# Optimization experiments

Measured on AMD Instinct MI355X. Metric: run time of the kernel, lower is better.

Reference implementation:

```python
import jax, jax.numpy as jnp
import numpy as np

C = 1024
H = 16
K = 2  # num_states
B, N = 4, 4096


def setup_inputs() -> dict:
    key = jax.random.key(0)
    ks_ = jax.random.split(key, 12)
    s = 1.0 / np.sqrt(C)
    inp = {
        "x": jax.random.normal(ks_[0], (B, N, C), dtype=jnp.float32),
        "Wq": jax.random.normal(ks_[1], (C, C), dtype=jnp.float32) * s,
        "bq": jnp.zeros((C,), dtype=jnp.float32),
        "Wk": jax.random.normal(ks_[2], (K, C, C), dtype=jnp.float32) * s,
        "bk": jnp.zeros((K, C), dtype=jnp.float32),
        "Wv": jax.random.normal(ks_[3], (K, C, C), dtype=jnp.float32) * s,
        "bv": jnp.zeros((K, C), dtype=jnp.float32),
        "Wo": jax.random.normal(ks_[4], (C, C), dtype=jnp.float32) * s,
        "bo": jnp.zeros((C,), dtype=jnp.float32),
        "ln_g": jnp.ones((C,), dtype=jnp.float32),
        "ln_b": jnp.zeros((C,), dtype=jnp.float32),
    }
    return inp


def _heads(t):
    # [..., n, (h d)] -> [..., h, n, d]
    shp = t.shape
    d = shp[-1] // H
    t = t.reshape(shp[:-1] + (H, d))
    return jnp.swapaxes(t, -2, -3)


def reference(x, Wq, bq, Wk, bk, Wv, bv, Wo, bo, ln_g, ln_b):
    dtype = x.dtype
    # residual single-layer projections (ResidualMLP with num_layers=-1)
    q = x + jnp.einsum('bnc,cd->bnd', x, Wq) + bq
    ks = x[None] + jnp.einsum('bnc,kcd->kbnd', x, Wk) + bk[:, None, None, :]
    vs = x[None] + jnp.einsum('bnc,kcd->kbnd', x, Wv) + bv[:, None, None, :]
    q = _heads(q)        # [b,h,n,d]
    ks = _heads(ks)      # [k,b,h,n,d]
    vs = _heads(vs)      # [k,b,h,n,d]
    scale = 1.0 / jnp.sqrt(jnp.asarray(N, dtype=jnp.float32))
    ks = ks.astype(jnp.float32) * scale
    vs = vs.astype(jnp.float32) * scale
    # per-state KV outer-products: [k,b,h,d,e]
    states = jnp.einsum('kbhnd,kbhne->kbhde', ks, vs)
    state = jnp.prod(states, axis=0)  # [b,h,d,e]
    out = jnp.einsum('bhnd,bhde->bhne', q.astype(jnp.float32), state)
    out = out.astype(dtype)
    # [b,h,n,d] -> [b,n,(h d)]
    out = jnp.swapaxes(out, 1, 2).reshape(x.shape[0], x.shape[1], C)
    # LayerNorm
    mu = jnp.mean(out, axis=-1, keepdims=True)
    var = jnp.var(out, axis=-1, keepdims=True)
    out = (out - mu) / jnp.sqrt(var + 1e-5) * ln_g + ln_b
    out = jnp.einsum('bnc,cd->bnd', out, Wo) + bo
    return out
```

## Files before the change

kernel.cpp:

```cpp
#include <hip/hip_runtime.h>
#include <hip/hip_bf16.h>

typedef __attribute__((ext_vector_type(8))) short bf16x8;
typedef __attribute__((ext_vector_type(4))) float f32x4;
typedef __attribute__((ext_vector_type(4))) short s16x4;

__device__ __forceinline__ short f2bf(float f) {
  union { float f; unsigned u; } v; v.f = f;
  unsigned r = v.u + 0x7fffu + ((v.u >> 16) & 1u);
  return (short)(r >> 16);
}

__device__ __forceinline__ float bf2f(short s) {
  union { float f; unsigned u; } v; v.u = ((unsigned)(unsigned short)s) << 16;
  return v.f;
}

#define GLD_LDS(g, l) __builtin_amdgcn_global_load_lds( \
    (const __attribute__((address_space(1))) void*)(g), \
    (__attribute__((address_space(3))) void*)(l), 16, 0, 0)

__global__ __launch_bounds__(256)
void convt_k(const float* __restrict__ x, short* __restrict__ xb,
             short* __restrict__ xbT, float* __restrict__ s) {
  __shared__ short tile[64][72];
  __shared__ float red[4][64];
  const int b = blockIdx.z;
  const int n0 = blockIdx.y * 64;
  const int c0 = blockIdx.x * 64;
  const int t = threadIdx.x;
  const int nl = t >> 4;
  const int c4 = (t & 15) << 2;
  const float* xp = x + ((size_t)b * 4096 + n0) * 1024 + c0;
#pragma unroll
  for (int i = 0; i < 4; ++i) {
    const int n = nl + 16 * i;
    const float4 v = *(const float4*)(xp + (size_t)n * 1024 + c4);
    s16x4 o;
    o[0] = f2bf(v.x); o[1] = f2bf(v.y); o[2] = f2bf(v.z); o[3] = f2bf(v.w);
    *(s16x4*)(&xb[((size_t)b * 4096 + n0 + n) * 1024 + c0 + c4]) = o;
    *(s16x4*)(&tile[n][c4]) = o;
  }
  __syncthreads();
  const int cll = t >> 4;
  const int n4 = (t & 15) << 2;
#pragma unroll
  for (int i = 0; i < 4; ++i) {
    const int c = cll + 16 * i;
    s16x4 o;
    o[0] = tile[n4 + 0][c]; o[1] = tile[n4 + 1][c];
    o[2] = tile[n4 + 2][c]; o[3] = tile[n4 + 3][c];
    *(s16x4*)(&xbT[((size_t)b * 1024 + c0 + c) * 4096 + n0 + n4]) = o;
  }
  const int part = t >> 6, col = t & 63;
  float cs = 0.f;
#pragma unroll
  for (int i = 0; i < 16; ++i) cs += bf2f(tile[part * 16 + i][col]);
  red[part][col] = cs;
  __syncthreads();
  if (part == 0)
    atomicAdd(&s[b * 1024 + c0 + col],
              red[0][col] + red[1][col] + red[2][col] + red[3][col]);
}

__global__ void twc_k(const float* __restrict__ Wq, const float* __restrict__ Wk,
                      const float* __restrict__ Wv, const float* __restrict__ Wo,
                      const float* __restrict__ lng, short* __restrict__ dst,
                      short* __restrict__ wqn) {
  __shared__ float tile[32][33];
  const int z = blockIdx.z;
  const float* src = (z == 0) ? Wq
                   : (z == 1) ? Wk
                   : (z == 2) ? (Wk + 1048576)
                   : (z == 3) ? Wv
                   : (z == 4) ? (Wv + 1048576)
                   : Wo;
  short* d = dst + (size_t)z * 1048576;
  const int tx = threadIdx.x, ty = threadIdx.y;
  const int c0 = blockIdx.y * 32, d0 = blockIdx.x * 32;
#pragma unroll
  for (int i = 0; i < 4; ++i) {
    const int cc = c0 + ty + i * 8;
    const float v = src[(size_t)cc * 1024 + d0 + tx];
    tile[ty + i * 8][tx] = v;
    if (z == 0)
      wqn[(size_t)cc * 1024 + d0 + tx] = f2bf(v + (cc == d0 + tx ? 1.0f : 0.0f));
  }
  __syncthreads();
#pragma unroll
  for (int i = 0; i < 4; ++i) {
    const int cc = c0 + tx;
    const int dd = d0 + ty + i * 8;
    float v = tile[tx][ty + i * 8];
    if (z < 5) {
      if (cc == dd) v += 1.0f;
    } else {
      v *= lng[cc];
    }
    d[(size_t)dd * 1024 + cc] = f2bf(v);
  }
}

__global__ __launch_bounds__(256)
void gemv_k(const short* __restrict__ wt, const float* __restrict__ s,
            float* __restrict__ u, float* __restrict__ w) {
  const int z = blockIdx.z, b = blockIdx.y;
  const int lane = threadIdx.x & 63, wid = threadIdx.x >> 6;
  const short* W = wt + ((size_t)(z + 1) << 20);
  const float* sb = s + b * 1024;
  float* outp = (z < 2) ? (u + (z * 4 + b) * 1024) : (w + ((z - 2) * 4 + b) * 1024);
#pragma unroll 1
  for (int it = 0; it < 16; ++it) {
    const int d = blockIdx.x * 64 + wid * 16 + it;
    const short* row = W + (size_t)d * 1024 + lane * 16;
    float acc = 0.f;
#pragma unroll
    for (int j = 0; j < 16; ++j) acc += bf2f(row[j]) * sb[lane * 16 + j];
#pragma unroll
    for (int o = 32; o > 0; o >>= 1) acc += __shfl_down(acc, o);
    if (lane == 0) outp[d] = acc;
  }
}

__global__ __launch_bounds__(256)
void ut_k(const float* __restrict__ Wo, const float* __restrict__ lng,
          const float* __restrict__ lnb, const float* __restrict__ bo,
          float* __restrict__ u, float* __restrict__ t) {
  const int dl = threadIdx.x & 63;
  const int dd = blockIdx.x * 64 + dl;
  const int part = threadIdx.x >> 6;
  float su = 0.f, st = 0.f;
  for (int c = part * 256; c < part * 256 + 256; ++c) {
    const float w = Wo[(size_t)c * 1024 + dd];
    su += lng[c] * w;
    st += lnb[c] * w;
  }
  __shared__ float rs[4][64], rt[4][64];
  rs[part][dl] = su; rt[part][dl] = st;
  __syncthreads();
  if (part == 0) {
    su = rs[0][dl] + rs[1][dl] + rs[2][dl] + rs[3][dl];
    st = rt[0][dl] + rt[1][dl] + rt[2][dl] + rt[3][dl];
    u[dd] = su;
    t[dd] = st + bo[dd];
  }
}

__global__ __launch_bounds__(512, 2)
void gram_k(const short* __restrict__ xbT, float* __restrict__ Pg) {
  extern __shared__ short lds[];
  const int tid = threadIdx.x;
  const int lane = tid & 63;
  const int wv = tid >> 6;
  const int wm = wv >> 2;
  const int wn = wv & 3;
  const int swz = ((blockIdx.x & 7) << 5) + (blockIdx.x >> 3);
  const int b = swz >> 6;
  const int kz = (swz >> 4) & 3;
  const int tl = swz & 15;
  const int bm0 = (tl >> 2) << 8, bn0 = (tl & 3) << 8;
  const int koff = kz << 10;
  const short* Ap = xbT + ((size_t)b << 22);
  float* po = Pg + ((size_t)((kz << 2) + b) << 20);

  const int lrow = ((lane >> 3) << 1) | ((lane >> 2) & 1);
  const int kc = ((lane & 3) ^ ((lane >> 3) & 3)) << 3;
  const int cl = lane & 15;
  const int khi = lane >> 4;

  f32x4 acc[8][4];
#pragma unroll
  for (int i = 0; i < 8; ++i)
#pragma unroll
    for (int j = 0; j < 4; ++j) acc[i][j] = f32x4{0.f, 0.f, 0.f, 0.f};

  auto stage = [&](int buf, int t) {
    const int k0 = koff + (t << 5) + kc;
    short* ab = lds + (buf << 14);
    short* bb = ab + 8192;
#pragma unroll
    for (int c = 0; c < 2; ++c) {
      const int un = wv * 2 + c;
      GLD_LDS(Ap + (size_t)(bm0 + (un << 4) + lrow) * 4096 + k0, ab + (un << 9));
      GLD_LDS(Ap + (size_t)(bn0 + (un << 4) + lrow) * 4096 + k0, bb + (un << 9));
    }
  };

  auto compute = [&](int buf) {
    const short* ab = lds + (buf << 14);
    const short* bb = ab + 8192;
    bf16x8 af[8], bfr[4];
#pragma unroll
    for (int i = 0; i < 8; ++i) {
      const int R = (wm << 7) + (i << 4) + cl;
      af[i] = *(const bf16x8*)(ab + (R << 5) + ((khi ^ ((R >> 1) & 3)) << 3));
    }
#pragma unroll
    for (int j = 0; j < 4; ++j) {
      const int C = (wn << 6) + (j << 4) + cl;
      bfr[j] = *(const bf16x8*)(bb + (C << 5) + ((khi ^ ((C >> 1) & 3)) << 3));
    }
#pragma unroll
    for (int i = 0; i < 8; ++i)
#pragma unroll
      for (int j = 0; j < 4; ++j)
        acc[i][j] = __builtin_amdgcn_mfma_f32_16x16x32_bf16(af[i], bfr[j], acc[i][j], 0, 0, 0);
  };

  stage(0, 0);
  stage(1, 1);
  asm volatile("s_waitcnt vmcnt(4)" ::: "memory");
  __builtin_amdgcn_s_barrier();
#pragma unroll 1
  for (int t = 0; t < 30; ++t) {
    stage((t + 2) & 3, t + 2);
    compute(t & 3);
    asm volatile("s_waitcnt vmcnt(4)" ::: "memory");
    __builtin_amdgcn_s_barrier();
  }
  compute(2);
  asm volatile("s_waitcnt vmcnt(0)" ::: "memory");
  __builtin_amdgcn_s_barrier();
  compute(3);

#pragma unroll
  for (int i = 0; i < 8; ++i)
#pragma unroll
    for (int j = 0; j < 4; ++j) {
      const int col = bn0 + (wn << 6) + (j << 4) + cl;
      const int rowb = bm0 + (wm << 7) + (i << 4) + (khi << 2);
#pragma unroll
      for (int r = 0; r < 4; ++r)
        po[(size_t)(rowb + r) * 1024 + col] = acc[i][j][r];
    }
}

__global__ __launch_bounds__(512, 2)
void oat_k(const short* __restrict__ xb, const short* __restrict__ Beff,
           const float* __restrict__ rq, short* __restrict__ oat,
           float* __restrict__ musum, float* __restrict__ sqsum) {
  extern __shared__ short lds[];
  const int tid = threadIdx.x;
  const int lane = tid & 63;
  const int wv = tid >> 6;
  const int wm = wv >> 2;
  const int wn = wv & 3;
  const int swz = ((blockIdx.x & 7) << 5) + (blockIdx.x >> 3);
  const int b = swz >> 6;
  const int tl = swz & 63;
  const int bm0 = (tl >> 2) << 8;
  const int bn0 = (tl & 3) << 8;
  const short* Ap = xb + ((size_t)b << 22);
  const short* Bp = Beff + ((size_t)b << 20);

  const int lrow = ((lane >> 3) << 1) | ((lane >> 2) & 1);
  const int kc = ((lane & 3) ^ ((lane >> 3) & 3)) << 3;
  const int cl = lane & 15;
  const int khi = lane >> 4;

  f32x4 acc[8][4];
#pragma unroll
  for (int i = 0; i < 8; ++i)
#pragma unroll
    for (int j = 0; j < 4; ++j) acc[i][j] = f32x4{0.f, 0.f, 0.f, 0.f};

  auto stage = [&](int buf, int t) {
    const int k0 = (t << 5) + kc;
    short* ab = lds + (buf << 14);
    short* bb = ab + 8192;
#pragma unroll
    for (int c = 0; c < 2; ++c) {
      const int un = wv * 2 + c;
      GLD_LDS(Ap + (size_t)(bm0 + (un << 4) + lrow) * 1024 + k0, ab + (un << 9));
      GLD_LDS(Bp + (size_t)(bn0 + (un << 4) + lrow) * 1024 + k0, bb + (un << 9));
    }
  };

  auto compute = [&](int buf) {
    const short* ab = lds + (buf << 14);
    const short* bb = ab + 8192;
    bf16x8 af[8], bfr[4];
#pragma unroll
    for (int i = 0; i < 8; ++i) {
      const int R = (wm << 7) + (i << 4) + cl;
      af[i] = *(const bf16x8*)(ab + (R << 5) + ((khi ^ ((R >> 1) & 3)) << 3));
    }
#pragma unroll
    for (int j = 0; j < 4; ++j) {
      const int C = (wn << 6) + (j << 4) + cl;
      bfr[j] = *(const bf16x8*)(bb + (C << 5) + ((khi ^ ((C >> 1) & 3)) << 3));
    }
#pragma unroll
    for (int i = 0; i < 8; ++i)
#pragma unroll
      for (int j = 0; j < 4; ++j)
        acc[i][j] = __builtin_amdgcn_mfma_f32_16x16x32_bf16(af[i], bfr[j], acc[i][j], 0, 0, 0);
  };

  stage(0, 0);
  stage(1, 1);
  asm volatile("s_waitcnt vmcnt(4)" ::: "memory");
  __builtin_amdgcn_s_barrier();
#pragma unroll 1
  for (int t = 0; t < 30; ++t) {
    stage((t + 2) & 3, t + 2);
    compute(t & 3);
    asm volatile("s_waitcnt vmcnt(4)" ::: "memory");
    __builtin_amdgcn_s_barrier();
  }
  compute(2);
  asm volatile("s_waitcnt vmcnt(0)" ::: "memory");
  __builtin_amdgcn_s_barrier();
  compute(3);

#pragma unroll
  for (int i = 0; i < 8; ++i) {
    const int rowb = bm0 + (wm << 7) + (i << 4) + (khi << 2);
    s16x4 pk[4];
#pragma unroll
    for (int j = 0; j < 4; ++j) {
      const int col = bn0 + (wn << 6) + (j << 4) + cl;
      const float rqc = rq[b * 1024 + col];
#pragma unroll
      for (int r = 0; r < 4; ++r) pk[j][r] = f2bf(acc[i][j][r] + rqc);
#pragma unroll
      for (int r = 0; r < 4; ++r)
        oat[(size_t)(b * 4096 + rowb + r) * 1024 + col] = pk[j][r];
    }
#pragma unroll
    for (int r = 0; r < 4; ++r) {
      float sv = 0.f, sq = 0.f;
#pragma unroll
      for (int j = 0; j < 4; ++j) {
        const float fv = bf2f(pk[j][r]);
        sv += fv; sq += fv * fv;
      }
#pragma unroll
      for (int m = 1; m < 16; m <<= 1) {
        sv += __shfl_xor(sv, m);
        sq += __shfl_xor(sq, m);
      }
      if (cl == 0) {
        atomicAdd(&musum[b * 4096 + rowb + r], sv);
        atomicAdd(&sqsum[b * 4096 + rowb + r], sq);
      }
    }
  }
}

__global__ __launch_bounds__(256)
void greduce_k(const float* __restrict__ Pg, short* __restrict__ G) {
  const int b = blockIdx.x >> 10;
  const int local = ((blockIdx.x & 1023) << 10) + (threadIdx.x << 2);
  float4 a = {0.f, 0.f, 0.f, 0.f};
#pragma unroll
  for (int kz = 0; kz < 4; ++kz) {
    const float4 v = *(const float4*)(Pg + (((size_t)((kz << 2) + b)) << 20) + local);
    a.x += v.x; a.y += v.y; a.z += v.z; a.w += v.w;
  }
  const float sc = 1.0f / 4096.0f;
  s16x4 o;
  o[0] = f2bf(a.x * sc); o[1] = f2bf(a.y * sc);
  o[2] = f2bf(a.z * sc); o[3] = f2bf(a.w * sc);
  *(s16x4*)(G + ((size_t)b << 20) + local) = o;
}

__global__ __launch_bounds__(256, 2)
void gemm128_k(const short* __restrict__ A, const short* __restrict__ Bt,
               short* __restrict__ out) {
  extern __shared__ short lds[];
  const int bid = blockIdx.x;
  const int swz = ((bid & 7) << 4) + (bid >> 3);
  const int bm0 = (swz >> 3) << 7;
  const int bn0 = (swz & 7) << 7;
  const short* Bp = Bt + ((size_t)blockIdx.y << 20);
  short* op = out + ((size_t)blockIdx.y << 21);
  const int tid = threadIdx.x, lane = tid & 63, wid = tid >> 6;
  const int wm = (wid >> 1) << 6, wn = (wid & 1) << 6;
  const int lrow = ((lane >> 3) << 1) | ((lane >> 2) & 1);
  const int kc = ((lane & 3) ^ ((lane >> 3) & 3)) << 3;
  const int cl = lane & 15, khi = lane >> 4;

  f32x4 acc[4][4];
#pragma unroll
  for (int i = 0; i < 4; ++i)
#pragma unroll
    for (int j = 0; j < 4; ++j) acc[i][j] = f32x4{0.f, 0.f, 0.f, 0.f};

  auto stage = [&](int buf, int t) {
    const int k0 = (t << 5) + kc;
    short* ab = lds + (buf << 13);
    short* bb = ab + 4096;
#pragma unroll
    for (int c = 0; c < 2; ++c) {
      const int un = wid * 2 + c;
      GLD_LDS(A + (size_t)(bm0 + (un << 4) + lrow) * 1024 + k0, ab + (un << 9));
      GLD_LDS(Bp + (size_t)(bn0 + (un << 4) + lrow) * 1024 + k0, bb + (un << 9));
    }
  };

  auto compute = [&](int buf) {
    const short* ab = lds + (buf << 13);
    const short* bb = ab + 4096;
    bf16x8 af[4], bfr[4];
#pragma unroll
    for (int i = 0; i < 4; ++i) {
      const int R = wm + (i << 4) + cl;
      af[i] = *(const bf16x8*)(ab + (R << 5) + ((khi ^ ((R >> 1) & 3)) << 3));
    }
#pragma unroll
    for (int j = 0; j < 4; ++j) {
      const int C = wn + (j << 4) + cl;
      bfr[j] = *(const bf16x8*)(bb + (C << 5) + ((khi ^ ((C >> 1) & 3)) << 3));
    }
#pragma unroll
    for (int i = 0; i < 4; ++i)
#pragma unroll
      for (int j = 0; j < 4; ++j)
        acc[i][j] = __builtin_amdgcn_mfma_f32_16x16x32_bf16(af[i], bfr[j], acc[i][j], 0, 0, 0);
  };

  stage(0, 0);
  stage(1, 1);
  asm volatile("s_waitcnt vmcnt(4)" ::: "memory");
  __builtin_amdgcn_s_barrier();
#pragma unroll 1
  for (int t = 0; t < 30; ++t) {
    stage((t + 2) & 3, t + 2);
    compute(t & 3);
    asm volatile("s_waitcnt vmcnt(4)" ::: "memory");
    __builtin_amdgcn_s_barrier();
  }
  compute(2);
  asm volatile("s_waitcnt vmcnt(0)" ::: "memory");
  __builtin_amdgcn_s_barrier();
  compute(3);

#pragma unroll
  for (int i = 0; i < 4; ++i)
#pragma unroll
    for (int j = 0; j < 4; ++j) {
      const int col = bn0 + wn + (j << 4) + cl;
      const int rowb = bm0 + wm + (i << 4) + (khi << 2);
#pragma unroll
      for (int r = 0; r < 4; ++r)
        op[(size_t)(rowb + r) * 1024 + col] = f2bf(acc[i][j][r]);
    }
}

__global__ __launch_bounds__(256)
void sw_k(const short* __restrict__ wt, const short* __restrict__ Tt,
          const float* __restrict__ u, const float* __restrict__ w,
          const float* __restrict__ bk, const float* __restrict__ bv,
          const short* __restrict__ wqn, const float* __restrict__ bq,
          short* __restrict__ Beff, float* __restrict__ rq) {
  __shared__ short Al[64 * 40];
  __shared__ short Bl[64 * 40];
  __shared__ short S[64][72];
  const int h = blockIdx.x & 15, b = blockIdx.x >> 4;
  const int tid = threadIdx.x, lane = tid & 63, wid = tid >> 6;
  const int srow = tid >> 2, sch = (tid & 3) << 3;
  const int cl = lane & 15, khi = lane >> 4;

  f32x4 acc2[2][4];
#pragma unroll
  for (int k = 0; k < 2; ++k)
#pragma unroll
    for (int j = 0; j < 4; ++j) acc2[k][j] = f32x4{0.f, 0.f, 0.f, 0.f};

#pragma unroll
  for (int k = 0; k < 2; ++k) {
    const short* Ap = wt + ((size_t)(1 + k) << 20) + ((size_t)(h * 64) << 10);
    const short* Bp = Tt + ((size_t)b << 21) + ((size_t)(k * 1024 + h * 64) << 10);
#pragma unroll 1
    for (int ns = 0; ns < 1024; ns += 32) {
      bf16x8 va = *(const bf16x8*)(Ap + ((size_t)srow << 10) + ns + sch);
      bf16x8 vb = *(const bf16x8*)(Bp + ((size_t)srow << 10) + ns + sch);
      __syncthreads();
      *(bf16x8*)(Al + srow * 40 + sch) = va;
      *(bf16x8*)(Bl + srow * 40 + sch) = vb;
      __syncthreads();
      bf16x8 a = *(const bf16x8*)(Al + (wid * 16 + cl) * 40 + (khi << 3));
#pragma unroll
      for (int j = 0; j < 4; ++j) {
        bf16x8 bb = *(const bf16x8*)(Bl + (j * 16 + cl) * 40 + (khi << 3));
        acc2[k][j] = __builtin_amdgcn_mfma_f32_16x16x32_bf16(a, bb, acc2[k][j], 0, 0, 0);
      }
    }
  }

  const int d0 = wid * 16 + (khi << 2);
  const float invN = 1.0f / 4096.0f;
#pragma unroll
  for (int j = 0; j < 4; ++j) {
    const int e = j * 16 + cl;
    s16x4 pk;
#pragma unroll
    for (int r = 0; r < 4; ++r) {
      const int d = d0 + r;
      float m[2];
#pragma unroll
      for (int k = 0; k < 2; ++k) {
        const float bkd = bk[k * 1024 + h * 64 + d];
        const float bve = bv[k * 1024 + h * 64 + e];
        const float ud = u[(k * 4 + b) * 1024 + h * 64 + d];
        const float we = w[(k * 4 + b) * 1024 + h * 64 + e];
        m[k] = acc2[k][j][r] + (ud * bve + bkd * we + 4096.f * bkd * bve) * invN;
      }
      pk[r] = f2bf(m[0] * m[1]);
    }
    *(s16x4*)(&S[e][d0]) = pk;
  }
  __syncthreads();

  if (wid == 0) {
    float acc = 0.f;
#pragma unroll 1
    for (int d = 0; d < 64; ++d) acc += bq[h * 64 + d] * bf2f(S[lane][d]);
    rq[b * 1024 + h * 64 + lane] = acc;
  }
  bf16x8 af[4][2];
#pragma unroll
  for (int mi = 0; mi < 4; ++mi)
#pragma unroll
    for (int kk = 0; kk < 2; ++kk)
      af[mi][kk] = *(const bf16x8*)(&S[mi * 16 + cl][kk * 32 + khi * 8]);
  const short* wq = wqn + h * 64;
  short* bdst = Beff + ((size_t)b << 20) + ((size_t)(h * 64) << 10);
#pragma unroll 1
  for (int nf = 0; nf < 16; ++nf) {
    const int c0 = wid * 256 + nf * 16;
    const bf16x8 bf0 = *(const bf16x8*)(wq + (size_t)(c0 + cl) * 1024 + khi * 8);
    const bf16x8 bf1 = *(const bf16x8*)(wq + (size_t)(c0 + cl) * 1024 + 32 + khi * 8);
    f32x4 a4[4];
#pragma unroll
    for (int mi = 0; mi < 4; ++mi) {
      a4[mi] = f32x4{0.f, 0.f, 0.f, 0.f};
      a4[mi] = __builtin_amdgcn_mfma_f32_16x16x32_bf16(af[mi][0], bf0, a4[mi], 0, 0, 0);
      a4[mi] = __builtin_amdgcn_mfma_f32_16x16x32_bf16(af[mi][1], bf1, a4[mi], 0, 0, 0);
    }
#pragma unroll
    for (int mi = 0; mi < 4; ++mi)
#pragma unroll
      for (int r = 0; r < 4; ++r)
        bdst[(size_t)(mi * 16 + khi * 4 + r) * 1024 + c0 + cl] = f2bf(a4[mi][r]);
  }
}

__global__ __launch_bounds__(512, 2)
void gemmo_k(const short* __restrict__ A, const short* __restrict__ WT,
             const float* __restrict__ musum, const float* __restrict__ sqsum,
             const float* __restrict__ uu, const float* __restrict__ tt,
             float* __restrict__ fout) {
  extern __shared__ short lds[];
  const int tid = threadIdx.x;
  const int lane = tid & 63;
  const int wv = tid >> 6;
  const int wm = wv >> 2;
  const int wn = wv & 3;
  const int swz = ((blockIdx.x & 7) << 5) + (blockIdx.x >> 3);
  const int bm0 = (swz >> 2) << 8;
  const int bn0 = (swz & 3) << 8;

  const int lrow = ((lane >> 3) << 1) | ((lane >> 2) & 1);
  const int kc = ((lane & 3) ^ ((lane >> 3) & 3)) << 3;
  const int cl = lane & 15;
  const int khi = lane >> 4;

  f32x4 acc[8][4];
#pragma unroll
  for (int i = 0; i < 8; ++i)
#pragma unroll
    for (int j = 0; j < 4; ++j) acc[i][j] = f32x4{0.f, 0.f, 0.f, 0.f};

  auto stage = [&](int buf, int t) {
    const int k0 = (t << 5) + kc;
    short* ab = lds + (buf << 14);
    short* bb = ab + 8192;
#pragma unroll
    for (int c = 0; c < 2; ++c) {
      const int un = wv * 2 + c;
      GLD_LDS(A + (size_t)(bm0 + (un << 4) + lrow) * 1024 + k0, ab + (un << 9));
      GLD_LDS(WT + (size_t)(bn0 + (un << 4) + lrow) * 1024 + k0, bb + (un << 9));
    }
  };

  auto compute = [&](int buf) {
    const short* ab = lds + (buf << 14);
    const short* bb = ab + 8192;
    bf16x8 af[8], bfr[4];
#pragma unroll
    for (int i = 0; i < 8; ++i) {
      const int R = (wm << 7) + (i << 4) + cl;
      af[i] = *(const bf16x8*)(ab + (R << 5) + ((khi ^ ((R >> 1) & 3)) << 3));
    }
#pragma unroll
    for (int j = 0; j < 4; ++j) {
      const int C = (wn << 6) + (j << 4) + cl;
      bfr[j] = *(const bf16x8*)(bb + (C << 5) + ((khi ^ ((C >> 1) & 3)) << 3));
    }
#pragma unroll
    for (int i = 0; i < 8; ++i)
#pragma unroll
      for (int j = 0; j < 4; ++j)
        acc[i][j] = __builtin_amdgcn_mfma_f32_16x16x32_bf16(af[i], bfr[j], acc[i][j], 0, 0, 0);
  };

  stage(0, 0);
  stage(1, 1);
  asm volatile("s_waitcnt vmcnt(4)" ::: "memory");
  __builtin_amdgcn_s_barrier();
#pragma unroll 1
  for (int t = 0; t < 30; ++t) {
    stage((t + 2) & 3, t + 2);
    compute(t & 3);
    asm volatile("s_waitcnt vmcnt(4)" ::: "memory");
    __builtin_amdgcn_s_barrier();
  }
  compute(2);
  asm volatile("s_waitcnt vmcnt(0)" ::: "memory");
  __builtin_amdgcn_s_barrier();
  compute(3);

#pragma unroll
  for (int i = 0; i < 8; ++i) {
    const int rowb = bm0 + (wm << 7) + (i << 4) + (khi << 2);
    const float4 ms = *(const float4*)(musum + rowb);
    const float4 qs = *(const float4*)(sqsum + rowb);
    float mu[4], rs[4];
    mu[0] = ms.x * (1.0f / 1024.0f); mu[1] = ms.y * (1.0f / 1024.0f);
    mu[2] = ms.z * (1.0f / 1024.0f); mu[3] = ms.w * (1.0f / 1024.0f);
    rs[0] = rsqrtf(fmaxf(qs.x * (1.0f / 1024.0f) - mu[0] * mu[0], 0.f) + 1e-5f);
    rs[1] = rsqrtf(fmaxf(qs.y * (1.0f / 1024.0f) - mu[1] * mu[1], 0.f) + 1e-5f);
    rs[2] = rsqrtf(fmaxf(qs.z * (1.0f / 1024.0f) - mu[2] * mu[2], 0.f) + 1e-5f);
    rs[3] = rsqrtf(fmaxf(qs.w * (1.0f / 1024.0f) - mu[3] * mu[3], 0.f) + 1e-5f);
#pragma unroll
    for (int j = 0; j < 4; ++j) {
      const int col = bn0 + (wn << 6) + (j << 4) + cl;
      const float uc = uu[col];
      const float tc = tt[col];
#pragma unroll
      for (int r = 0; r < 4; ++r)
        fout[(size_t)(rowb + r) * 1024 + col] = rs[r] * (acc[i][j][r] - mu[r] * uc) + tc;
    }
  }
}

extern "C" void kernel_launch(void* const* d_in, const int* in_sizes, int n_in,
                              void* d_out, int out_size, void* d_ws, size_t ws_size,
                              hipStream_t stream) {
  const float* x = (const float*)d_in[0];
  const float* Wq = (const float*)d_in[1];
  const float* bq = (const float*)d_in[2];
  const float* Wk = (const float*)d_in[3];
  const float* bk = (const float*)d_in[4];
  const float* Wv = (const float*)d_in[5];
  const float* bv = (const float*)d_in[6];
  const float* Wo = (const float*)d_in[7];
  const float* bo = (const float*)d_in[8];
  const float* lng = (const float*)d_in[9];
  const float* lnb = (const float*)d_in[10];

  char* ws = (char*)d_ws;
  short* xb = (short*)(ws + 0);
  short* wt = (short*)(ws + 33554432);
  short* wqn = (short*)(ws + 46137344);
  short* Beff = (short*)(ws + 48234496);
  float* rq = (float*)(ws + 56623104);
  float* musum = (float*)(ws + 56639488);
  float* sqsum = (float*)(ws + 56705024);
  float* s = (float*)(ws + 56770560);
  float* u = (float*)(ws + 56786944);
  float* w = (float*)(ws + 56819712);
  float* uu = (float*)(ws + 56852480);
  float* tt = (float*)(ws + 56856576);
  short* xbT = (short*)(ws + 79691776);
  short* Gt = (short*)(ws + 113246208);
  short* Tt = (short*)(ws + 121634816);
  float* Pg = (float*)(ws + 143351808);
  short* oat = xbT;

  hipMemsetAsync(musum, 0, 147456, stream);
  convt_k<<<dim3(16, 64, 4), 256, 0, stream>>>(x, xb, xbT, s);
  twc_k<<<dim3(32, 32, 6), dim3(32, 8), 0, stream>>>(Wq, Wk, Wv, Wo, lng, wt, wqn);
  gemv_k<<<dim3(16, 4, 4), 256, 0, stream>>>(wt, s, u, w);
  ut_k<<<16, 256, 0, stream>>>(Wo, lng, lnb, bo, uu, tt);

  gram_k<<<256, 512, 131072, stream>>>(xbT, Pg);
  greduce_k<<<4096, 256, 0, stream>>>(Pg, Gt);
  gemm128_k<<<dim3(128, 4), 256, 65536, stream>>>(wt + 3145728, Gt, Tt);
  sw_k<<<64, 256, 0, stream>>>(wt, Tt, u, w, bk, bv, wqn, bq, Beff, rq);

  oat_k<<<256, 512, 131072, stream>>>(xb, Beff, rq, oat, musum, sqsum);
  gemmo_k<<<256, 512, 131072, stream>>>(oat, wt + 5242880, musum, sqsum, uu, tt,
                                        (float*)d_out);
}
```

Before: 271.6 us.

## Exploit Gram symmetry: compute upper-triangle tiles only, mirror in reduction

The Gram kernel now computes only the 10 upper-triangular 256x256 tiles per batch instead of all 16. Each tile's K dimension is split into 6 uneven chunks, giving 240 blocks. A new reduction kernel sums the 6 partials, converts to bf16, writes the tile, and uses an LDS transpose to write the mirrored lower tile. This removes about 37% of the Gram MFMA work and balances the grid against the CU count. The cost is an uneven split-K and a larger partial-sum footprint, plus a transpose in the reduction.

New measurement: 262.8 us. 1.03x faster.

```diff
diff --git a/kernel.cpp b/kernel.cpp
--- a/kernel.cpp
+++ b/kernel.cpp
@@ -154,14 +154,19 @@
   const int wv = tid >> 6;
   const int wm = wv >> 2;
   const int wn = wv & 3;
-  const int swz = ((blockIdx.x & 7) << 5) + (blockIdx.x >> 3);
-  const int b = swz >> 6;
-  const int kz = (swz >> 4) & 3;
-  const int tl = swz & 15;
-  const int bm0 = (tl >> 2) << 8, bn0 = (tl & 3) << 8;
-  const int koff = kz << 10;
+
+  const int g = blockIdx.x;
+  const int p = g / 6, sp = g - p * 6;
+  const int b = p / 10;
+  int t = p - b * 10, ti = 0;
+  while (t >= 4 - ti) { t -= 4 - ti; ++ti; }
+  const int tj = ti + t;
+  const int kst[7] = {0, 21, 42, 64, 85, 106, 128};
+  const int bm0 = ti << 8, bn0 = tj << 8;
+  const int koff = kst[sp] << 5;
+  const int nt = kst[sp + 1] - kst[sp];
   const short* Ap = xbT + ((size_t)b << 22);
-  float* po = Pg + ((size_t)((kz << 2) + b) << 20);
+  float* po = Pg + ((size_t)g << 16);
 
   const int lrow = ((lane >> 3) << 1) | ((lane >> 2) & 1);
   const int kc = ((lane & 3) ^ ((lane >> 3) & 3)) << 3;
@@ -174,8 +179,8 @@
 #pragma unroll
     for (int j = 0; j < 4; ++j) acc[i][j] = f32x4{0.f, 0.f, 0.f, 0.f};
 
-  auto stage = [&](int buf, int t) {
-    const int k0 = koff + (t << 5) + kc;
+  auto stage = [&](int buf, int t2) {
+    const int k0 = koff + (t2 << 5) + kc;
     short* ab = lds + (buf << 14);
     short* bb = ab + 8192;
 #pragma unroll
@@ -202,6 +207,144 @@
     }
 #pragma unroll
     for (int i = 0; i < 8; ++i)
+#pragma unroll
+      for (int j = 0; j < 4; ++j)
+        acc[i][j] = __builtin_amdgcn_mfma_f32_16x16x32_bf16(af[i], bfr[j], acc[i][j], 0, 0, 0);
+  };
+
+  stage(0, 0);
+  stage(1, 1);
+  asm volatile("s_waitcnt vmcnt(4)" ::: "memory");
+  __builtin_amdgcn_s_barrier();
+#pragma unroll 1
+  for (int t2 = 0; t2 < nt - 2; ++t2) {
+    stage((t2 + 2) & 3, t2 + 2);
+    compute(t2 & 3);
+    asm volatile("s_waitcnt vmcnt(4)" ::: "memory");
+    __builtin_amdgcn_s_barrier();
+  }
+  compute((nt - 2) & 3);
+  asm volatile("s_waitcnt vmcnt(0)" ::: "memory");
+  __builtin_amdgcn_s_barrier();
+  compute((nt - 1) & 3);
+
+#pragma unroll
+  for (int i = 0; i < 8; ++i)
+#pragma unroll
+    for (int j = 0; j < 4; ++j) {
+      const int col = (wn << 6) + (j << 4) + cl;
+      const int rowb = (wm << 7) + (i << 4) + (khi << 2);
+#pragma unroll
+      for (int r = 0; r < 4; ++r)
+        po[(size_t)(rowb + r) * 256 + col] = acc[i][j][r];
+    }
+}
+
+__global__ __launch_bounds__(256)
+void gred6_k(const float* __restrict__ Pg, short* __restrict__ G) {
+  __shared__ short tile[64][72];
+  const int bid = blockIdx.x;
+  const int p = bid >> 4;
+  const int st = bid & 15;
+  const int b = p / 10;
+  int t = p - b * 10, ti = 0;
+  while (t >= 4 - ti) { t -= 4 - ti; ++ti; }
+  const int tj = ti + t;
+  const int sr = st >> 2, sc = st & 3;
+  const int r = threadIdx.x >> 2;
+  const int c0 = (threadIdx.x & 3) << 4;
+  float acc[16];
+#pragma unroll
+  for (int qq = 0; qq < 16; ++qq) acc[qq] = 0.f;
+#pragma unroll
+  for (int s = 0; s < 6; ++s) {
+    const float* base = Pg + ((size_t)(p * 6 + s) << 16)
+                      + (size_t)(sr * 64 + r) * 256 + sc * 64 + c0;
+#pragma unroll
+    for (int q4 = 0; q4 < 4; ++q4) {
+      const float4 v = ((const float4*)base)[q4];
+      acc[q4 * 4 + 0] += v.x; acc[q4 * 4 + 1] += v.y;
+      acc[q4 * 4 + 2] += v.z; acc[q4 * 4 + 3] += v.w;
+    }
+  }
+  const float scf = 1.0f / 4096.0f;
+  short* gb = G + ((size_t)b << 20);
+  const int row = ti * 256 + sr * 64 + r;
+  const int colb = tj * 256 + sc * 64 + c0;
+#pragma unroll
+  for (int q4 = 0; q4 < 4; ++q4) {
+    s16x4 o;
+#pragma unroll
+    for (int e = 0; e < 4; ++e) {
+      o[e] = f2bf(acc[q4 * 4 + e] * scf);
+      tile[r][c0 + q4 * 4 + e] = o[e];
+    }
+    *(s16x4*)(gb + (size_t)row * 1024 + colb + q4 * 4) = o;
+  }
+  __syncthreads();
+  if (ti != tj) {
+    const int row2 = tj * 256 + sc * 64 + r;
+    const int col2 = ti * 256 + sr * 64 + c0;
+#pragma unroll
+    for (int q4 = 0; q4 < 4; ++q4) {
+      s16x4 o;
+#pragma unroll
+      for (int e = 0; e < 4; ++e) o[e] = tile[c0 + q4 * 4 + e][r];
+      *(s16x4*)(gb + (size_t)row2 * 1024 + col2 + q4 * 4) = o;
+    }
+  }
+}
+
+__global__ __launch_bounds__(256, 2)
+void gemm128_k(const short* __restrict__ A, const short* __restrict__ Bt,
+               short* __restrict__ out) {
+  extern __shared__ short lds[];
+  const int bid = blockIdx.x;
+  const int swz = ((bid & 7) << 4) + (bid >> 3);
+  const int bm0 = (swz >> 3) << 7;
+  const int bn0 = (swz & 7) << 7;
+  const short* Bp = Bt + ((size_t)blockIdx.y << 20);
+  short* op = out + ((size_t)blockIdx.y << 21);
+  const int tid = threadIdx.x, lane = tid & 63, wid = tid >> 6;
+  const int wm = (wid >> 1) << 6, wn = (wid & 1) << 6;
+  const int lrow = ((lane >> 3) << 1) | ((lane >> 2) & 1);
+  const int kc = ((lane & 3) ^ ((lane >> 3) & 3)) << 3;
+  const int cl = lane & 15, khi = lane >> 4;
+
+  f32x4 acc[4][4];
+#pragma unroll
+  for (int i = 0; i < 4; ++i)
+#pragma unroll
+    for (int j = 0; j < 4; ++j) acc[i][j] = f32x4{0.f, 0.f, 0.f, 0.f};
+
+  auto stage = [&](int buf, int t) {
+    const int k0 = (t << 5) + kc;
+    short* ab = lds + (buf << 13);
+    short* bb = ab + 4096;
+#pragma unroll
+    for (int c = 0; c < 2; ++c) {
+      const int un = wid * 2 + c;
+      GLD_LDS(A + (size_t)(bm0 + (un << 4) + lrow) * 1024 + k0, ab + (un << 9));
+      GLD_LDS(Bp + (size_t)(bn0 + (un << 4) + lrow) * 1024 + k0, bb + (un << 9));
+    }
+  };
+
+  auto compute = [&](int buf) {
+    const short* ab = lds + (buf << 13);
+    const short* bb = ab + 4096;
+    bf16x8 af[4], bfr[4];
+#pragma unroll
+    for (int i = 0; i < 4; ++i) {
+      const int R = wm + (i << 4) + cl;
+      af[i] = *(const bf16x8*)(ab + (R << 5) + ((khi ^ ((R >> 1) & 3)) << 3));
+    }
+#pragma unroll
+    for (int j = 0; j < 4; ++j) {
+      const int C = wn + (j << 4) + cl;
+      bfr[j] = *(const bf16x8*)(bb + (C << 5) + ((khi ^ ((C >> 1) & 3)) << 3));
+    }
+#pragma unroll
+    for (int i = 0; i < 4; ++i)
 #pragma unroll
       for (int j = 0; j < 4; ++j)
         acc[i][j] = __builtin_amdgcn_mfma_f32_16x16x32_bf16(af[i], bfr[j], acc[i][j], 0, 0, 0);
@@ -224,15 +367,114 @@
   compute(3);
 
 #pragma unroll
-  for (int i = 0; i < 8; ++i)
+  for (int i = 0; i < 4; ++i)
 #pragma unroll
     for (int j = 0; j < 4; ++j) {
-      const int col = bn0 + (wn << 6) + (j << 4) + cl;
-      const int rowb = bm0 + (wm << 7) + (i << 4) + (khi << 2);
+      const int col = bn0 + wn + (j << 4) + cl;
+      const int rowb = bm0 + wm + (i << 4) + (khi << 2);
 #pragma unroll
       for (int r = 0; r < 4; ++r)
-        po[(size_t)(rowb + r) * 1024 + col] = acc[i][j][r];
-    }
+        op[(size_t)(rowb + r) * 1024 + col] = f2bf(acc[i][j][r]);
+    }
+}
+
+__global__ __launch_bounds__(256)
+void sw_k(const short* __restrict__ wt, const short* __restrict__ Tt,
+          const float* __restrict__ u, const float* __restrict__ w,
+          const float* __restrict__ bk, const float* __restrict__ bv,
+          const short* __restrict__ wqn, const float* __restrict__ bq,
+          short* __restrict__ Beff, float* __restrict__ rq) {
+  __shared__ short Al[64 * 40];
+  __shared__ short Bl[64 * 40];
+  __shared__ short S[64][72];
+  const int h = blockIdx.x & 15, b = blockIdx.x >> 4;
+  const int tid = threadIdx.x, lane = tid & 63, wid = tid >> 6;
+  const int srow = tid >> 2, sch = (tid & 3) << 3;
+  const int cl = lane & 15, khi = lane >> 4;
+
+  f32x4 acc2[2][4];
+#pragma unroll
+  for (int k = 0; k < 2; ++k)
+#pragma unroll
+    for (int j = 0; j < 4; ++j) acc2[k][j] = f32x4{0.f, 0.f, 0.f, 0.f};
+
+#pragma unroll
+  for (int k = 0; k < 2; ++k) {
+    const short* Ap = wt + ((size_t)(1 + k) << 20) + ((size_t)(h * 64) << 10);
+    const short* Bp = Tt + ((size_t)b << 21) + ((size_t)(k * 1024 + h * 64) << 10);
+#pragma unroll 1
+    for (int ns = 0; ns < 1024; ns += 32) {
+      bf16x8 va = *(const bf16x8*)(Ap + ((size_t)srow << 10) + ns + sch);
+      bf16x8 vb = *(const bf16x8*)(Bp + ((size_t)srow << 10) + ns + sch);
+      __syncthreads();
+      *(bf16x8*)(Al + srow * 40 + sch) = va;
+      *(bf16x8*)(Bl + srow * 40 + sch) = vb;
+      __syncthreads();
+      bf16x8 a = *(const bf16x8*)(Al + (wid * 16 + cl) * 40 + (khi << 3));
+#pragma unroll
+      for (int j = 0; j < 4; ++j) {
+        bf16x8 bb = *(const bf16x8*)(Bl + (j * 16 + cl) * 40 + (khi << 3));
+        acc2[k][j] = __builtin_amdgcn_mfma_f32_16x16x32_bf16(a, bb, acc2[k][j], 0, 0, 0);
+      }
+    }
+  }
+
+  const int d0 = wid * 16 + (khi << 2);
+  const float invN = 1.0f / 4096.0f;
+#pragma unroll
+  for (int j = 0; j < 4; ++j) {
+    const int e = j * 16 + cl;
+    s16x4 pk;
+#pragma unroll
+    for (int r = 0; r < 4; ++r) {
+      const int d = d0 + r;
+      float m[2];
+#pragma unroll
+      for (int k = 0; k < 2; ++k) {
+        const float bkd = bk[k * 1024 + h * 64 + d];
+        const float bve = bv[k * 1024 + h * 64 + e];
+        const float ud = u[(k * 4 + b) * 1024 + h * 64 + d];
+        const float we = w[(k * 4 + b) * 1024 + h * 64 + e];
+        m[k] = acc2[k][j][r] + (ud * bve + bkd * we + 4096.f * bkd * bve) * invN;
+      }
+      pk[r] = f2bf(m[0] * m[1]);
+    }
+    *(s16x4*)(&S[e][d0]) = pk;
+  }
+  __syncthreads();
+
+  if (wid == 0) {
+    float acc = 0.f;
+#pragma unroll 1
+    for (int d = 0; d < 64; ++d) acc += bq[h * 64 + d] * bf2f(S[lane][d]);
+    rq[b * 1024 + h * 64 + lane] = acc;
+  }
+  bf16x8 af[4][2];
+#pragma unroll
+  for (int mi = 0; mi < 4; ++mi)
+#pragma unroll
+    for (int kk = 0; kk < 2; ++kk)
+      af[mi][kk] = *(const bf16x8*)(&S[mi * 16 + cl][kk * 32 + khi * 8]);
+  const short* wq = wqn + h * 64;
+  short* bdst = Beff + ((size_t)b << 20) + ((size_t)(h * 64) << 10);
+#pragma unroll 1
+  for (int nf = 0; nf < 16; ++nf) {
+    const int c0 = wid * 256 + nf * 16;
+    const bf16x8 bf0 = *(const bf16x8*)(wq + (size_t)(c0 + cl) * 1024 + khi * 8);
+    const bf16x8 bf1 = *(const bf16x8*)(wq + (size_t)(c0 + cl) * 1024 + 32 + khi * 8);
+    f32x4 a4[4];
+#pragma unroll
+    for (int mi = 0; mi < 4; ++mi) {
+      a4[mi] = f32x4{0.f, 0.f, 0.f, 0.f};
+      a4[mi] = __builtin_amdgcn_mfma_f32_16x16x32_bf16(af[mi][0], bf0, a4[mi], 0, 0, 0);
+      a4[mi] = __builtin_amdgcn_mfma_f32_16x16x32_bf16(af[mi][1], bf1, a4[mi], 0, 0, 0);
+    }
+#pragma unroll
+    for (int mi = 0; mi < 4; ++mi)
+#pragma unroll
+      for (int r = 0; r < 4; ++r)
+        bdst[(size_t)(mi * 16 + khi * 4 + r) * 1024 + c0 + cl] = f2bf(a4[mi][r]);
+  }
 }
 
 __global__ __launch_bounds__(512, 2)
@@ -348,205 +590,6 @@
   }
 }
 
-__global__ __launch_bounds__(256)
-void greduce_k(const float* __restrict__ Pg, short* __restrict__ G) {
-  const int b = blockIdx.x >> 10;
-  const int local = ((blockIdx.x & 1023) << 10) + (threadIdx.x << 2);
-  float4 a = {0.f, 0.f, 0.f, 0.f};
-#pragma unroll
-  for (int kz = 0; kz < 4; ++kz) {
-    const float4 v = *(const float4*)(Pg + (((size_t)((kz << 2) + b)) << 20) + local);
-    a.x += v.x; a.y += v.y; a.z += v.z; a.w += v.w;
-  }
-  const float sc = 1.0f / 4096.0f;
-  s16x4 o;
-  o[0] = f2bf(a.x * sc); o[1] = f2bf(a.y * sc);
-  o[2] = f2bf(a.z * sc); o[3] = f2bf(a.w * sc);
-  *(s16x4*)(G + ((size_t)b << 20) + local) = o;
-}
-
-__global__ __launch_bounds__(256, 2)
-void gemm128_k(const short* __restrict__ A, const short* __restrict__ Bt,
-               short* __restrict__ out) {
-  extern __shared__ short lds[];
-  const int bid = blockIdx.x;
-  const int swz = ((bid & 7) << 4) + (bid >> 3);
-  const int bm0 = (swz >> 3) << 7;
-  const int bn0 = (swz & 7) << 7;
-  const short* Bp = Bt + ((size_t)blockIdx.y << 20);
-  short* op = out + ((size_t)blockIdx.y << 21);
-  const int tid = threadIdx.x, lane = tid & 63, wid = tid >> 6;
-  const int wm = (wid >> 1) << 6, wn = (wid & 1) << 6;
-  const int lrow = ((lane >> 3) << 1) | ((lane >> 2) & 1);
-  const int kc = ((lane & 3) ^ ((lane >> 3) & 3)) << 3;
-  const int cl = lane & 15, khi = lane >> 4;
-
-  f32x4 acc[4][4];
-#pragma unroll
-  for (int i = 0; i < 4; ++i)
-#pragma unroll
-    for (int j = 0; j < 4; ++j) acc[i][j] = f32x4{0.f, 0.f, 0.f, 0.f};
-
-  auto stage = [&](int buf, int t) {
-    const int k0 = (t << 5) + kc;
-    short* ab = lds + (buf << 13);
-    short* bb = ab + 4096;
-#pragma unroll
-    for (int c = 0; c < 2; ++c) {
-      const int un = wid * 2 + c;
-      GLD_LDS(A + (size_t)(bm0 + (un << 4) + lrow) * 1024 + k0, ab + (un << 9));
-      GLD_LDS(Bp + (size_t)(bn0 + (un << 4) + lrow) * 1024 + k0, bb + (un << 9));
-    }
-  };
-
-  auto compute = [&](int buf) {
-    const short* ab = lds + (buf << 13);
-    const short* bb = ab + 4096;
-    bf16x8 af[4], bfr[4];
-#pragma unroll
-    for (int i = 0; i < 4; ++i) {
-      const int R = wm + (i << 4) + cl;
-      af[i] = *(const bf16x8*)(ab + (R << 5) + ((khi ^ ((R >> 1) & 3)) << 3));
-    }
-#pragma unroll
-    for (int j = 0; j < 4; ++j) {
-      const int C = wn + (j << 4) + cl;
-      bfr[j] = *(const bf16x8*)(bb + (C << 5) + ((khi ^ ((C >> 1) & 3)) << 3));
-    }
-#pragma unroll
-    for (int i = 0; i < 4; ++i)
-#pragma unroll
-      for (int j = 0; j < 4; ++j)
-        acc[i][j] = __builtin_amdgcn_mfma_f32_16x16x32_bf16(af[i], bfr[j], acc[i][j], 0, 0, 0);
-  };
-
-  stage(0, 0);
-  stage(1, 1);
-  asm volatile("s_waitcnt vmcnt(4)" ::: "memory");
-  __builtin_amdgcn_s_barrier();
-#pragma unroll 1
-  for (int t = 0; t < 30; ++t) {
-    stage((t + 2) & 3, t + 2);
-    compute(t & 3);
-    asm volatile("s_waitcnt vmcnt(4)" ::: "memory");
-    __builtin_amdgcn_s_barrier();
-  }
-  compute(2);
-  asm volatile("s_waitcnt vmcnt(0)" ::: "memory");
-  __builtin_amdgcn_s_barrier();
-  compute(3);
-
-#pragma unroll
-  for (int i = 0; i < 4; ++i)
-#pragma unroll
-    for (int j = 0; j < 4; ++j) {
-      const int col = bn0 + wn + (j << 4) + cl;
-      const int rowb = bm0 + wm + (i << 4) + (khi << 2);
-#pragma unroll
-      for (int r = 0; r < 4; ++r)
-        op[(size_t)(rowb + r) * 1024 + col] = f2bf(acc[i][j][r]);
-    }
-}
-
-__global__ __launch_bounds__(256)
-void sw_k(const short* __restrict__ wt, const short* __restrict__ Tt,
-          const float* __restrict__ u, const float* __restrict__ w,
-          const float* __restrict__ bk, const float* __restrict__ bv,
-          const short* __restrict__ wqn, const float* __restrict__ bq,
-          short* __restrict__ Beff, float* __restrict__ rq) {
-  __shared__ short Al[64 * 40];
-  __shared__ short Bl[64 * 40];
-  __shared__ short S[64][72];
-  const int h = blockIdx.x & 15, b = blockIdx.x >> 4;
-  const int tid = threadIdx.x, lane = tid & 63, wid = tid >> 6;
-  const int srow = tid >> 2, sch = (tid & 3) << 3;
-  const int cl = lane & 15, khi = lane >> 4;
-
-  f32x4 acc2[2][4];
-#pragma unroll
-  for (int k = 0; k < 2; ++k)
-#pragma unroll
-    for (int j = 0; j < 4; ++j) acc2[k][j] = f32x4{0.f, 0.f, 0.f, 0.f};
-
-#pragma unroll
-  for (int k = 0; k < 2; ++k) {
-    const short* Ap = wt + ((size_t)(1 + k) << 20) + ((size_t)(h * 64) << 10);
-    const short* Bp = Tt + ((size_t)b << 21) + ((size_t)(k * 1024 + h * 64) << 10);
-#pragma unroll 1
-    for (int ns = 0; ns < 1024; ns += 32) {
-      bf16x8 va = *(const bf16x8*)(Ap + ((size_t)srow << 10) + ns + sch);
-      bf16x8 vb = *(const bf16x8*)(Bp + ((size_t)srow << 10) + ns + sch);
-      __syncthreads();
-      *(bf16x8*)(Al + srow * 40 + sch) = va;
-      *(bf16x8*)(Bl + srow * 40 + sch) = vb;
-      __syncthreads();
-      bf16x8 a = *(const bf16x8*)(Al + (wid * 16 + cl) * 40 + (khi << 3));
-#pragma unroll
-      for (int j = 0; j < 4; ++j) {
-        bf16x8 bb = *(const bf16x8*)(Bl + (j * 16 + cl) * 40 + (khi << 3));
-        acc2[k][j] = __builtin_amdgcn_mfma_f32_16x16x32_bf16(a, bb, acc2[k][j], 0, 0, 0);
-      }
-    }
-  }
-
-  const int d0 = wid * 16 + (khi << 2);
-  const float invN = 1.0f / 4096.0f;
-#pragma unroll
-  for (int j = 0; j < 4; ++j) {
-    const int e = j * 16 + cl;
-    s16x4 pk;
-#pragma unroll
-    for (int r = 0; r < 4; ++r) {
-      const int d = d0 + r;
-      float m[2];
-#pragma unroll
-      for (int k = 0; k < 2; ++k) {
-        const float bkd = bk[k * 1024 + h * 64 + d];
-        const float bve = bv[k * 1024 + h * 64 + e];
-        const float ud = u[(k * 4 + b) * 1024 + h * 64 + d];
-        const float we = w[(k * 4 + b) * 1024 + h * 64 + e];
-        m[k] = acc2[k][j][r] + (ud * bve + bkd * we + 4096.f * bkd * bve) * invN;
-      }
-      pk[r] = f2bf(m[0] * m[1]);
-    }
-    *(s16x4*)(&S[e][d0]) = pk;
-  }
-  __syncthreads();
-
-  if (wid == 0) {
-    float acc = 0.f;
-#pragma unroll 1
-    for (int d = 0; d < 64; ++d) acc += bq[h * 64 + d] * bf2f(S[lane][d]);
-    rq[b * 1024 + h * 64 + lane] = acc;
-  }
-  bf16x8 af[4][2];
-#pragma unroll
-  for (int mi = 0; mi < 4; ++mi)
-#pragma unroll
-    for (int kk = 0; kk < 2; ++kk)
-      af[mi][kk] = *(const bf16x8*)(&S[mi * 16 + cl][kk * 32 + khi * 8]);
-  const short* wq = wqn + h * 64;
-  short* bdst = Beff + ((size_t)b << 20) + ((size_t)(h * 64) << 10);
-#pragma unroll 1
-  for (int nf = 0; nf < 16; ++nf) {
-    const int c0 = wid * 256 + nf * 16;
-    const bf16x8 bf0 = *(const bf16x8*)(wq + (size_t)(c0 + cl) * 1024 + khi * 8);
-    const bf16x8 bf1 = *(const bf16x8*)(wq + (size_t)(c0 + cl) * 1024 + 32 + khi * 8);
-    f32x4 a4[4];
-#pragma unroll
-    for (int mi = 0; mi < 4; ++mi) {
-      a4[mi] = f32x4{0.f, 0.f, 0.f, 0.f};
-      a4[mi] = __builtin_amdgcn_mfma_f32_16x16x32_bf16(af[mi][0], bf0, a4[mi], 0, 0, 0);
-      a4[mi] = __builtin_amdgcn_mfma_f32_16x16x32_bf16(af[mi][1], bf1, a4[mi], 0, 0, 0);
-    }
-#pragma unroll
-    for (int mi = 0; mi < 4; ++mi)
-#pragma unroll
-      for (int r = 0; r < 4; ++r)
-        bdst[(size_t)(mi * 16 + khi * 4 + r) * 1024 + c0 + cl] = f2bf(a4[mi][r]);
-  }
-}
-
 __global__ __launch_bounds__(512, 2)
 void gemmo_k(const short* __restrict__ A, const short* __restrict__ WT,
              const float* __restrict__ musum, const float* __restrict__ sqsum,
@@ -667,27 +710,27 @@
   short* wqn = (short*)(ws + 46137344);
   short* Beff = (short*)(ws + 48234496);
   float* rq = (float*)(ws + 56623104);
-  float* musum = (float*)(ws + 56639488);
-  float* sqsum = (float*)(ws + 56705024);
-  float* s = (float*)(ws + 56770560);
-  float* u = (float*)(ws + 56786944);
-  float* w = (float*)(ws + 56819712);
-  float* uu = (float*)(ws + 56852480);
-  float* tt = (float*)(ws + 56856576);
+  float* u = (float*)(ws + 56639488);
+  float* w = (float*)(ws + 56672256);
+  float* uu = (float*)(ws + 56705024);
+  float* tt = (float*)(ws + 56709120);
+  float* s = (float*)(ws + 56713216);
+  float* musum = (float*)(ws + 56729600);
+  float* sqsum = (float*)(ws + 56795136);
   short* xbT = (short*)(ws + 79691776);
   short* Gt = (short*)(ws + 113246208);
   short* Tt = (short*)(ws + 121634816);
   float* Pg = (float*)(ws + 143351808);
   short* oat = xbT;
 
-  hipMemsetAsync(musum, 0, 147456, stream);
+  hipMemsetAsync(s, 0, 147456, stream);
   convt_k<<<dim3(16, 64, 4), 256, 0, stream>>>(x, xb, xbT, s);
   twc_k<<<dim3(32, 32, 6), dim3(32, 8), 0, stream>>>(Wq, Wk, Wv, Wo, lng, wt, wqn);
   gemv_k<<<dim3(16, 4, 4), 256, 0, stream>>>(wt, s, u, w);
   ut_k<<<16, 256, 0, stream>>>(Wo, lng, lnb, bo, uu, tt);
 
-  gram_k<<<256, 512, 131072, stream>>>(xbT, Pg);
-  greduce_k<<<4096, 256, 0, stream>>>(Pg, Gt);
+  gram_k<<<240, 512, 131072, stream>>>(xbT, Pg);
+  gred6_k<<<640, 256, 0, stream>>>(Pg, Gt);
   gemm128_k<<<dim3(128, 4), 256, 65536, stream>>>(wt + 3145728, Gt, Tt);
   sw_k<<<64, 256, 0, stream>>>(wt, Tt, u, w, bk, bv, wqn, bq, Beff, rq);
 
```
